# Optimization experiments

Hardware: AMD Instinct MI355X
Metric: run time of the kernel (lower is better)

Reference implementation:

```python
import jax, jax.numpy as jnp
import numpy as np

NUM_HEADS = 16

def setup_inputs() -> dict:
    key = jax.random.key(0)
    k1, k2, k3, k4 = jax.random.split(key, 4)
    B, N, C = 4, 2048, 1024
    x = jax.random.normal(k1, (B, N, C), dtype=jnp.float32)
    xpos = jax.random.randint(k2, (B, N), 0, 2048, dtype=jnp.int64)
    Wqkv = jax.random.normal(k3, (C, 3 * C), dtype=jnp.float32) * (C ** -0.5)
    Wproj = jax.random.normal(k4, (C, C), dtype=jnp.float32) * (C ** -0.5)
    bproj = jnp.zeros((C,), dtype=jnp.float32)
    return {"x": x, "xpos": xpos, "Wqkv": Wqkv, "Wproj": Wproj, "bproj": bproj}

def reference(x, xpos, Wqkv, Wproj, bproj):
    # rope is None in this configuration, so xpos is unused (matches torch default path).
    B, N, C = x.shape
    H = NUM_HEADS
    Dh = C // H
    scale = Dh ** -0.5
    qkv = jnp.einsum('bnc,cd->bnd', x, Wqkv)              # [B, N, 3C]
    qkv = qkv.reshape(B, N, 3, H, Dh)
    q, k, v = qkv[:, :, 0], qkv[:, :, 1], qkv[:, :, 2]    # [B, N, H, Dh]
    scores = jnp.einsum('bnhd,bmhd->bhnm', q, k) * scale  # [B, H, N, N]
    attn = jax.nn.softmax(scores, axis=-1)
    out = jnp.einsum('bhnm,bmhd->bnhd', attn, v)          # [B, N, H, Dh]
    out = out.reshape(B, N, C)
    return jnp.einsum('bnc,cd->bnd', out, Wproj) + bproj
```

## Files before the change

kernel.cpp:

```cpp
#include <hip/hip_runtime.h>
#include <stdint.h>

#define DEVINL __device__ __forceinline__

typedef __bf16 bf16x8 __attribute__((ext_vector_type(8)));
typedef float f32x4 __attribute__((ext_vector_type(4)));
typedef float f32x16 __attribute__((ext_vector_type(16)));
typedef uint32_t u32x4 __attribute__((ext_vector_type(4)));

DEVINL uint16_t f2bf(float f) {
    uint32_t u = __builtin_bit_cast(uint32_t, f);
    uint32_t r = (u + 0x7FFFu + ((u >> 16) & 1u)) >> 16;
    return (uint16_t)r;
}

DEVINL bf16x8 ld8(const uint16_t* p) {
    u32x4 v = *(const u32x4*)p;
    return __builtin_bit_cast(bf16x8, v);
}

DEVINL void gload16(const void* g, void* l) {
    __builtin_amdgcn_global_load_lds(
        (const __attribute__((address_space(1))) uint32_t*)g,
        (__attribute__((address_space(3))) uint32_t*)l, 16, 0, 0);
}

DEVINL uint32_t cvtpk(float lo, float hi) {
    uint32_t r;
    asm("v_cvt_pk_bf16_f32 %0, %1, %2" : "=v"(r) : "v"(lo), "v"(hi));
    return r;
}

DEVINL float exp2_fast(float x) {
    float r;
    asm("v_exp_f32 %0, %1" : "=v"(r) : "v"(x));
    return r;
}

DEVINL void transW_body(const float* __restrict__ W, uint16_t* __restrict__ WT,
                        int Nn, int n0, int k0, int tid, uint16_t* t) {
#pragma unroll
    for (int i = 0; i < 4; ++i) {
        int c = tid + i * 256;
        int kr = c >> 4, nc = c & 15;
        float4 v = *(const float4*)(W + (size_t)(k0 + kr) * Nn + n0 + nc * 4);
        t[(nc * 4 + 0) * 65 + kr] = f2bf(v.x);
        t[(nc * 4 + 1) * 65 + kr] = f2bf(v.y);
        t[(nc * 4 + 2) * 65 + kr] = f2bf(v.z);
        t[(nc * 4 + 3) * 65 + kr] = f2bf(v.w);
    }
    __syncthreads();
#pragma unroll
    for (int i = 0; i < 2; ++i) {
        int c = tid + i * 256;
        int nr = c >> 3, kc = c & 7;
        union { uint16_t u[8]; u32x4 v; } o;
#pragma unroll
        for (int j = 0; j < 8; ++j) o.u[j] = t[nr * 65 + kc * 8 + j];
        *(u32x4*)(WT + (size_t)(n0 + nr) * 1024 + k0 + kc * 8) = o.v;
    }
}

__global__ void k_prep(const float* __restrict__ x, uint16_t* __restrict__ xb,
                       const float* __restrict__ Wqkv, uint16_t* __restrict__ wqkvT,
                       const float* __restrict__ Wproj, uint16_t* __restrict__ wprojT) {
    __shared__ uint16_t t[64 * 65];
    int bid = blockIdx.x;
    int tid = threadIdx.x;
    if (bid < 4096) {
        int i = bid * 256 + tid;
        const float4* src = (const float4*)x + (size_t)i * 2;
        float4 a = src[0], b = src[1];
        union { uint16_t u[8]; u32x4 v; } o;
        o.u[0] = f2bf(a.x); o.u[1] = f2bf(a.y); o.u[2] = f2bf(a.z); o.u[3] = f2bf(a.w);
        o.u[4] = f2bf(b.x); o.u[5] = f2bf(b.y); o.u[6] = f2bf(b.z); o.u[7] = f2bf(b.w);
        ((u32x4*)xb)[i] = o.v;
    } else if (bid < 4864) {
        int idx = bid - 4096;
        transW_body(Wqkv, wqkvT, 3072, (idx % 48) * 64, (idx / 48) * 64, tid, t);
    } else {
        int idx = bid - 4864;
        transW_body(Wproj, wprojT, 1024, (idx % 16) * 64, (idx / 16) * 64, tid, t);
    }
}

__global__ void k_transV(const uint16_t* __restrict__ vn, uint16_t* __restrict__ vt) {
    __shared__ uint16_t t[64 * 65];
    int bh = blockIdx.y;
    int n0 = blockIdx.x * 64;
    int tid = threadIdx.x;
#pragma unroll
    for (int i = 0; i < 2; ++i) {
        int c = tid + i * 256;
        int n = c >> 3, dc = c & 7;
        u32x4 vv = *(const u32x4*)(vn + ((size_t)bh * 2048 + n0 + n) * 64 + dc * 8);
        union { u32x4 v4; uint16_t u[8]; } in; in.v4 = vv;
#pragma unroll
        for (int j = 0; j < 8; ++j) t[(dc * 8 + j) * 65 + n] = in.u[j];
    }
    __syncthreads();
#pragma unroll
    for (int i = 0; i < 2; ++i) {
        int c = tid + i * 256;
        int dh = c >> 3, nc = c & 7;
        union { uint16_t u[8]; u32x4 v4; } o;
#pragma unroll
        for (int j = 0; j < 8; ++j) o.u[j] = t[dh * 65 + nc * 8 + j];
        *(u32x4*)(vt + ((size_t)bh * 64 + dh) * 2048 + n0 + nc * 8) = o.v4;
    }
}

template <int MODE>
__global__ __launch_bounds__(256) void k_gemm(
    const uint16_t* __restrict__ A, const uint16_t* __restrict__ BT,
    const float* __restrict__ bias,
    uint16_t* __restrict__ qo, uint16_t* __restrict__ ko, uint16_t* __restrict__ vo,
    float* __restrict__ out) {
    __shared__ uint16_t a_lds[128 * 64];
    __shared__ uint16_t b_lds[128 * 64];
    int tid = threadIdx.x;
    int w = tid >> 6, l = tid & 63;
    int l15 = l & 15, l4 = l >> 4;
    int m0 = blockIdx.y * 128, n0 = blockIdx.x * 128;
    int wr = w >> 1, wc = w & 1;
    f32x4 acc[4][4] = {};

    for (int kt = 0; kt < 16; ++kt) {
#pragma unroll
        for (int i = 0; i < 4; ++i) {
            int c = i * 256 + w * 64 + l;
            int row = c >> 3, slot = c & 7;
            int kc = slot ^ (row & 7);
            gload16(A + (size_t)(m0 + row) * 1024 + kt * 64 + kc * 8,
                    a_lds + (size_t)(i * 256 + w * 64) * 8);
            gload16(BT + (size_t)(n0 + row) * 1024 + kt * 64 + kc * 8,
                    b_lds + (size_t)(i * 256 + w * 64) * 8);
        }
        __syncthreads();
#pragma unroll
        for (int kkk = 0; kkk < 2; ++kkk) {
            bf16x8 af[4], bfr[4];
#pragma unroll
            for (int i = 0; i < 4; ++i) {
                int row = wr * 64 + i * 16 + l15;
                af[i] = ld8(a_lds + row * 64 + ((kkk * 4 + l4) ^ (row & 7)) * 8);
                int rowb = wc * 64 + i * 16 + l15;
                bfr[i] = ld8(b_lds + rowb * 64 + ((kkk * 4 + l4) ^ (rowb & 7)) * 8);
            }
#pragma unroll
            for (int i = 0; i < 4; ++i)
#pragma unroll
                for (int j = 0; j < 4; ++j)
                    acc[i][j] = __builtin_amdgcn_mfma_f32_16x16x32_bf16(
                        af[i], bfr[j], acc[i][j], 0, 0, 0);
        }
        __syncthreads();
    }

    if constexpr (MODE == 0) {
#pragma unroll
        for (int i = 0; i < 4; ++i)
#pragma unroll
            for (int j = 0; j < 4; ++j) {
                int d = n0 + wc * 64 + j * 16 + l15;
                int s = d >> 10, h = (d >> 6) & 15, dh = d & 63;
                float sc = (s == 0) ? 0.18033688011112042f : 1.0f;
#pragma unroll
                for (int r = 0; r < 4; ++r) {
                    int m = m0 + wr * 64 + i * 16 + l4 * 4 + r;
                    int b = m >> 11, n = m & 2047;
                    int bh = b * 16 + h;
                    uint16_t val = f2bf(acc[i][j][r] * sc);
                    if (s == 1) {
                        ko[(size_t)bh * 131072 + (size_t)(n >> 6) * 4096 +
                           (dh >> 3) * 512 + (n & 63) * 8 + (dh & 7)] = val;
                    } else {
                        uint16_t* dst0 = (s == 0) ? qo : vo;
                        dst0[((size_t)bh * 2048 + n) * 64 + dh] = val;
                    }
                }
            }
    } else {
#pragma unroll
        for (int j = 0; j < 4; ++j) {
            int d = n0 + wc * 64 + j * 16 + l15;
            float bv = bias[d];
#pragma unroll
            for (int i = 0; i < 4; ++i)
#pragma unroll
                for (int r = 0; r < 4; ++r) {
                    int m = m0 + wr * 64 + i * 16 + l4 * 4 + r;
                    out[(size_t)m * 1024 + d] = acc[i][j][r] + bv;
                }
        }
    }
}

__global__ __launch_bounds__(256) void k_attn(
    const uint16_t* __restrict__ q, const uint16_t* __restrict__ kf_,
    const uint16_t* __restrict__ vt, uint16_t* __restrict__ o) {
    __shared__ uint16_t v_lds[2][64 * 64];
    int tid = threadIdx.x;
    int w = tid >> 6, l = tid & 63;
    int l31 = l & 31, g = l >> 5;
    int bid = blockIdx.x;
    int slot = bid >> 3;
    int bh = (bid & 7) * 8 + (slot >> 4);
    int qt = slot & 15;
    int qrow = qt * 128 + w * 32 + l31;
    const uint16_t* qb = q + ((size_t)bh * 2048 + qrow) * 64;
    const uint16_t* vbase = vt + (size_t)bh * 64 * 2048;
    const uint16_t* kfb = kf_ + (size_t)bh * 131072 + g * 512 + l31 * 8;

    bf16x8 qf[4];
#pragma unroll
    for (int kv = 0; kv < 4; ++kv) qf[kv] = ld8(qb + kv * 16 + g * 8);

    int c0 = w * 128 + l;
    int rr0 = c0 >> 3, sl0 = c0 & 7;
    int kc0 = sl0 ^ (rr0 & 7);
    int rr1 = rr0 + 8, kc1 = sl0 ^ (rr1 & 7);
    const uint16_t* vp0 = vbase + (size_t)rr0 * 2048 + kc0 * 8;
    const uint16_t* vp1 = vbase + (size_t)rr1 * 2048 + kc1 * 8;
    uint16_t* vd0 = v_lds[0] + w * 1024;
    uint16_t* vd1 = v_lds[1] + w * 1024;

    bf16x8 kr[8];
    auto loadK = [&](int t) {
        const uint16_t* p = kfb + (size_t)t * 4096;
        kr[0] = ld8(p);        kr[1] = ld8(p + 1024);
        kr[2] = ld8(p + 2048); kr[3] = ld8(p + 3072);
        kr[4] = ld8(p + 256);  kr[5] = ld8(p + 1280);
        kr[6] = ld8(p + 2304); kr[7] = ld8(p + 3328);
    };
    auto stageV = [&](uint16_t* vd) {
        gload16(vp0, vd); gload16(vp1, vd + 512);
        vp0 += 64; vp1 += 64;
    };

    f32x16 oa[2] = {};
    float lsum = 0.f;

    loadK(0);
    stageV(vd0);

    auto body = [&](int t, const uint16_t* vb, uint16_t* vdn) {
        asm volatile("s_barrier" ::: "memory");

        bf16x8 pfrag[4];
#pragma unroll
        for (int j = 0; j < 2; ++j) {
            f32x16 stj = {};
            __builtin_amdgcn_s_setprio(1);
#pragma unroll
            for (int kv = 0; kv < 4; ++kv)
                stj = __builtin_amdgcn_mfma_f32_32x32x16_bf16(kr[j * 4 + kv], qf[kv], stj, 0, 0, 0);
            __builtin_amdgcn_s_setprio(0);
            if (j == 1 && t < 31) {
                loadK(t + 1);
                stageV(vdn);
            }
#pragma unroll
            for (int h = 0; h < 2; ++h) {
                float e[8];
#pragma unroll
                for (int jj = 0; jj < 8; ++jj) e[jj] = exp2_fast(stj[h * 8 + jj]);
                lsum += ((e[0] + e[1]) + (e[2] + e[3])) + ((e[4] + e[5]) + (e[6] + e[7]));
                uint32_t a0 = cvtpk(e[0], e[1]), a1 = cvtpk(e[2], e[3]);
                uint32_t b0 = cvtpk(e[4], e[5]), b1 = cvtpk(e[6], e[7]);
                auto r0 = __builtin_amdgcn_permlane32_swap(a0, b0, false, false);
                auto r1 = __builtin_amdgcn_permlane32_swap(a1, b1, false, false);
                u32x4 f;
                f[0] = r0[0]; f[1] = r1[0]; f[2] = r0[1]; f[3] = r1[1];
                pfrag[j * 2 + h] = __builtin_bit_cast(bf16x8, f);
            }
        }

        if (t < 31) asm volatile("s_waitcnt vmcnt(10)\n\ts_barrier" ::: "memory");
        else        asm volatile("s_waitcnt vmcnt(0)\n\ts_barrier" ::: "memory");

        __builtin_amdgcn_s_setprio(1);
#pragma unroll
        for (int kv = 0; kv < 4; ++kv) {
#pragma unroll
            for (int dt = 0; dt < 2; ++dt) {
                int dh = dt * 32 + l31;
                bf16x8 vf = ld8(vb + dh * 64 + ((2 * kv + g) ^ (dh & 7)) * 8);
                oa[dt] = __builtin_amdgcn_mfma_f32_32x32x16_bf16(vf, pfrag[kv], oa[dt], 0, 0, 0);
            }
        }
        __builtin_amdgcn_s_setprio(0);
    };

    for (int kt = 0; kt < 32; kt += 2) {
        body(kt,     v_lds[0], vd1);
        body(kt + 1, v_lds[1], vd0);
    }

    float ltot = lsum + __shfl_xor(lsum, 32, 64);
    float inv = 1.0f / ltot;
    int b = bh >> 4, h = bh & 15;
    uint16_t* ob = o + ((size_t)(b * 2048 + qrow)) * 1024 + h * 64;
#pragma unroll
    for (int dt = 0; dt < 2; ++dt)
#pragma unroll
        for (int rq = 0; rq < 4; ++rq) {
            union { uint16_t u[4]; uint2 v; } pk;
#pragma unroll
            for (int rr = 0; rr < 4; ++rr) pk.u[rr] = f2bf(oa[dt][rq * 4 + rr] * inv);
            int dh0 = dt * 32 + rq * 8 + g * 4;
            *(uint2*)(ob + dh0) = pk.v;
        }
}

extern "C" void kernel_launch(void* const* d_in, const int* in_sizes, int n_in,
                              void* d_out, int out_size, void* d_ws, size_t ws_size,
                              hipStream_t stream) {
    const float* x     = (const float*)d_in[0];
    const float* Wqkv  = (const float*)d_in[2];
    const float* Wproj = (const float*)d_in[3];
    const float* bproj = (const float*)d_in[4];
    float* out = (float*)d_out;

    char* ws = (char*)d_ws;
    uint16_t* xb     = (uint16_t*)(ws);
    uint16_t* wqkvT  = (uint16_t*)(ws + 16777216);
    uint16_t* wprojT = (uint16_t*)(ws + 23068672);
    uint16_t* qws    = (uint16_t*)(ws + 25165824);
    uint16_t* kws    = (uint16_t*)(ws + 41943040);
    uint16_t* vT     = (uint16_t*)(ws + 58720256);
    uint16_t* vnat   = (uint16_t*)(ws + 75497472);
    uint16_t* attnout = xb;

    k_prep<<<dim3(5120), dim3(256), 0, stream>>>(x, xb, Wqkv, wqkvT, Wproj, wprojT);
    k_gemm<0><<<dim3(24, 64), dim3(256), 0, stream>>>(xb, wqkvT, nullptr, qws, kws, vnat, nullptr);
    k_transV<<<dim3(32, 64), dim3(256), 0, stream>>>(vnat, vT);
    k_attn<<<dim3(1024), dim3(256), 0, stream>>>(qws, kws, vT, attnout);
    k_gemm<1><<<dim3(8, 64), dim3(256), 0, stream>>>(attnout, wprojT, bproj, nullptr, nullptr, nullptr, out);
}
```

Before: 212.6 us.

## Write V in MFMA fragment layout from QKV GEMM and drop V transpose kernel

The QKV GEMM epilogue now writes V directly in a fragment-friendly layout with packed 8-byte stores, which removes the separate k_transV launch and its extra round-trip through memory. The attention kernel no longer stages V through LDS or uses barriers. Each wave loads K and V fragments straight from global memory into registers and walks 32-key tiles with a per-wave staggered start offset. In exchange, cross-wave reuse of V through shared memory is lost, so global and L2 traffic rises, and each tile's loads are less deeply prefetched.

Result: slower. 219.4 us (+3.2%).

```diff
diff --git a/kernel.cpp b/kernel.cpp
--- a/kernel.cpp
+++ b/kernel.cpp
@@ -84,32 +84,6 @@
     }
 }
 
-__global__ void k_transV(const uint16_t* __restrict__ vn, uint16_t* __restrict__ vt) {
-    __shared__ uint16_t t[64 * 65];
-    int bh = blockIdx.y;
-    int n0 = blockIdx.x * 64;
-    int tid = threadIdx.x;
-#pragma unroll
-    for (int i = 0; i < 2; ++i) {
-        int c = tid + i * 256;
-        int n = c >> 3, dc = c & 7;
-        u32x4 vv = *(const u32x4*)(vn + ((size_t)bh * 2048 + n0 + n) * 64 + dc * 8);
-        union { u32x4 v4; uint16_t u[8]; } in; in.v4 = vv;
-#pragma unroll
-        for (int j = 0; j < 8; ++j) t[(dc * 8 + j) * 65 + n] = in.u[j];
-    }
-    __syncthreads();
-#pragma unroll
-    for (int i = 0; i < 2; ++i) {
-        int c = tid + i * 256;
-        int dh = c >> 3, nc = c & 7;
-        union { uint16_t u[8]; u32x4 v4; } o;
-#pragma unroll
-        for (int j = 0; j < 8; ++j) o.u[j] = t[dh * 65 + nc * 8 + j];
-        *(u32x4*)(vt + ((size_t)bh * 64 + dh) * 2048 + n0 + nc * 8) = o.v4;
-    }
-}
-
 template <int MODE>
 __global__ __launch_bounds__(256) void k_gemm(
     const uint16_t* __restrict__ A, const uint16_t* __restrict__ BT,
@@ -165,18 +139,29 @@
                 int d = n0 + wc * 64 + j * 16 + l15;
                 int s = d >> 10, h = (d >> 6) & 15, dh = d & 63;
                 float sc = (s == 0) ? 0.18033688011112042f : 1.0f;
-#pragma unroll
-                for (int r = 0; r < 4; ++r) {
-                    int m = m0 + wr * 64 + i * 16 + l4 * 4 + r;
+                if (s == 2) {
+                    int m = m0 + wr * 64 + i * 16 + l4 * 4;
                     int b = m >> 11, n = m & 2047;
                     int bh = b * 16 + h;
-                    uint16_t val = f2bf(acc[i][j][r] * sc);
-                    if (s == 1) {
-                        ko[(size_t)bh * 131072 + (size_t)(n >> 6) * 4096 +
-                           (dh >> 3) * 512 + (n & 63) * 8 + (dh & 7)] = val;
-                    } else {
-                        uint16_t* dst0 = (s == 0) ? qo : vo;
-                        dst0[((size_t)bh * 2048 + n) * 64 + dh] = val;
+                    union { uint16_t u[4]; uint2 v2; } pk;
+#pragma unroll
+                    for (int r = 0; r < 4; ++r) pk.u[r] = f2bf(acc[i][j][r]);
+                    size_t addr = (size_t)bh * 131072 + (size_t)(n >> 5) * 2048 +
+                                  ((n & 31) >> 3) * 512 + dh * 8 + (n & 7);
+                    *(uint2*)(vo + addr) = pk.v2;
+                } else {
+#pragma unroll
+                    for (int r = 0; r < 4; ++r) {
+                        int m = m0 + wr * 64 + i * 16 + l4 * 4 + r;
+                        int b = m >> 11, n = m & 2047;
+                        int bh = b * 16 + h;
+                        uint16_t val = f2bf(acc[i][j][r] * sc);
+                        if (s == 1) {
+                            ko[(size_t)bh * 131072 + (size_t)(n >> 6) * 4096 +
+                               (dh >> 3) * 512 + (n & 63) * 8 + (dh & 7)] = val;
+                        } else {
+                            qo[((size_t)bh * 2048 + n) * 64 + dh] = val;
+                        }
                     }
                 }
             }
@@ -198,8 +183,7 @@
 
 __global__ __launch_bounds__(256) void k_attn(
     const uint16_t* __restrict__ q, const uint16_t* __restrict__ kf_,
-    const uint16_t* __restrict__ vt, uint16_t* __restrict__ o) {
-    __shared__ uint16_t v_lds[2][64 * 64];
+    const uint16_t* __restrict__ vf_, uint16_t* __restrict__ o) {
     int tid = threadIdx.x;
     int w = tid >> 6, l = tid & 63;
     int l31 = l & 31, g = l >> 5;
@@ -209,92 +193,65 @@
     int qt = slot & 15;
     int qrow = qt * 128 + w * 32 + l31;
     const uint16_t* qb = q + ((size_t)bh * 2048 + qrow) * 64;
-    const uint16_t* vbase = vt + (size_t)bh * 64 * 2048;
     const uint16_t* kfb = kf_ + (size_t)bh * 131072 + g * 512 + l31 * 8;
+    const uint16_t* vfb = vf_ + (size_t)bh * 131072 + g * 512 + l31 * 8;
 
     bf16x8 qf[4];
 #pragma unroll
     for (int kv = 0; kv < 4; ++kv) qf[kv] = ld8(qb + kv * 16 + g * 8);
 
-    int c0 = w * 128 + l;
-    int rr0 = c0 >> 3, sl0 = c0 & 7;
-    int kc0 = sl0 ^ (rr0 & 7);
-    int rr1 = rr0 + 8, kc1 = sl0 ^ (rr1 & 7);
-    const uint16_t* vp0 = vbase + (size_t)rr0 * 2048 + kc0 * 8;
-    const uint16_t* vp1 = vbase + (size_t)rr1 * 2048 + kc1 * 8;
-    uint16_t* vd0 = v_lds[0] + w * 1024;
-    uint16_t* vd1 = v_lds[1] + w * 1024;
-
-    bf16x8 kr[8];
+    bf16x8 kr[4];
+    bf16x8 vr[4];
+    f32x16 oa[2] = {};
+    float lsum = 0.f;
+
     auto loadK = [&](int t) {
-        const uint16_t* p = kfb + (size_t)t * 4096;
+        const uint16_t* p = kfb + (t >> 1) * 4096 + (t & 1) * 256;
         kr[0] = ld8(p);        kr[1] = ld8(p + 1024);
         kr[2] = ld8(p + 2048); kr[3] = ld8(p + 3072);
-        kr[4] = ld8(p + 256);  kr[5] = ld8(p + 1280);
-        kr[6] = ld8(p + 2304); kr[7] = ld8(p + 3328);
     };
-    auto stageV = [&](uint16_t* vd) {
-        gload16(vp0, vd); gload16(vp1, vd + 512);
-        vp0 += 64; vp1 += 64;
+    auto loadV = [&](int t) {
+        const uint16_t* p = vfb + t * 2048;
+        vr[0] = ld8(p);        vr[1] = ld8(p + 1024);
+        vr[2] = ld8(p + 256);  vr[3] = ld8(p + 1280);
     };
 
-    f32x16 oa[2] = {};
-    float lsum = 0.f;
-
-    loadK(0);
-    stageV(vd0);
-
-    auto body = [&](int t, const uint16_t* vb, uint16_t* vdn) {
-        asm volatile("s_barrier" ::: "memory");
-
-        bf16x8 pfrag[4];
-#pragma unroll
-        for (int j = 0; j < 2; ++j) {
-            f32x16 stj = {};
+    int start = w * 16;
+    loadK(start);
+    loadV(start);
+    int t = start;
+
+    for (int it = 0; it < 64; ++it) {
+        int tn = (t + 1) & 63;
+
+        f32x16 stj = {};
+        __builtin_amdgcn_s_setprio(1);
+#pragma unroll
+        for (int kv = 0; kv < 4; ++kv)
+            stj = __builtin_amdgcn_mfma_f32_32x32x16_bf16(kr[kv], qf[kv], stj, 0, 0, 0);
+        __builtin_amdgcn_s_setprio(0);
+        loadK(tn);
+
+#pragma unroll
+        for (int h = 0; h < 2; ++h) {
+            float e[8];
+#pragma unroll
+            for (int jj = 0; jj < 8; ++jj) e[jj] = exp2_fast(stj[h * 8 + jj]);
+            lsum += ((e[0] + e[1]) + (e[2] + e[3])) + ((e[4] + e[5]) + (e[6] + e[7]));
+            uint32_t a0 = cvtpk(e[0], e[1]), a1 = cvtpk(e[2], e[3]);
+            uint32_t b0 = cvtpk(e[4], e[5]), b1 = cvtpk(e[6], e[7]);
+            auto r0 = __builtin_amdgcn_permlane32_swap(a0, b0, false, false);
+            auto r1 = __builtin_amdgcn_permlane32_swap(a1, b1, false, false);
+            u32x4 f;
+            f[0] = r0[0]; f[1] = r1[0]; f[2] = r0[1]; f[3] = r1[1];
+            bf16x8 pf = __builtin_bit_cast(bf16x8, f);
             __builtin_amdgcn_s_setprio(1);
-#pragma unroll
-            for (int kv = 0; kv < 4; ++kv)
-                stj = __builtin_amdgcn_mfma_f32_32x32x16_bf16(kr[j * 4 + kv], qf[kv], stj, 0, 0, 0);
+            oa[0] = __builtin_amdgcn_mfma_f32_32x32x16_bf16(vr[h],     pf, oa[0], 0, 0, 0);
+            oa[1] = __builtin_amdgcn_mfma_f32_32x32x16_bf16(vr[2 + h], pf, oa[1], 0, 0, 0);
             __builtin_amdgcn_s_setprio(0);
-            if (j == 1 && t < 31) {
-                loadK(t + 1);
-                stageV(vdn);
-            }
-#pragma unroll
-            for (int h = 0; h < 2; ++h) {
-                float e[8];
-#pragma unroll
-                for (int jj = 0; jj < 8; ++jj) e[jj] = exp2_fast(stj[h * 8 + jj]);
-                lsum += ((e[0] + e[1]) + (e[2] + e[3])) + ((e[4] + e[5]) + (e[6] + e[7]));
-                uint32_t a0 = cvtpk(e[0], e[1]), a1 = cvtpk(e[2], e[3]);
-                uint32_t b0 = cvtpk(e[4], e[5]), b1 = cvtpk(e[6], e[7]);
-                auto r0 = __builtin_amdgcn_permlane32_swap(a0, b0, false, false);
-                auto r1 = __builtin_amdgcn_permlane32_swap(a1, b1, false, false);
-                u32x4 f;
-                f[0] = r0[0]; f[1] = r1[0]; f[2] = r0[1]; f[3] = r1[1];
-                pfrag[j * 2 + h] = __builtin_bit_cast(bf16x8, f);
-            }
-        }
-
-        if (t < 31) asm volatile("s_waitcnt vmcnt(10)\n\ts_barrier" ::: "memory");
-        else        asm volatile("s_waitcnt vmcnt(0)\n\ts_barrier" ::: "memory");
-
-        __builtin_amdgcn_s_setprio(1);
-#pragma unroll
-        for (int kv = 0; kv < 4; ++kv) {
-#pragma unroll
-            for (int dt = 0; dt < 2; ++dt) {
-                int dh = dt * 32 + l31;
-                bf16x8 vf = ld8(vb + dh * 64 + ((2 * kv + g) ^ (dh & 7)) * 8);
-                oa[dt] = __builtin_amdgcn_mfma_f32_32x32x16_bf16(vf, pfrag[kv], oa[dt], 0, 0, 0);
-            }
-        }
-        __builtin_amdgcn_s_setprio(0);
-    };
-
-    for (int kt = 0; kt < 32; kt += 2) {
-        body(kt,     v_lds[0], vd1);
-        body(kt + 1, v_lds[1], vd0);
+        }
+        loadV(tn);
+        t = tn;
     }
 
     float ltot = lsum + __shfl_xor(lsum, 32, 64);
@@ -328,13 +285,11 @@
     uint16_t* wprojT = (uint16_t*)(ws + 23068672);
     uint16_t* qws    = (uint16_t*)(ws + 25165824);
     uint16_t* kws    = (uint16_t*)(ws + 41943040);
-    uint16_t* vT     = (uint16_t*)(ws + 58720256);
-    uint16_t* vnat   = (uint16_t*)(ws + 75497472);
+    uint16_t* vfr    = (uint16_t*)(ws + 58720256);
     uint16_t* attnout = xb;
 
     k_prep<<<dim3(5120), dim3(256), 0, stream>>>(x, xb, Wqkv, wqkvT, Wproj, wprojT);
-    k_gemm<0><<<dim3(24, 64), dim3(256), 0, stream>>>(xb, wqkvT, nullptr, qws, kws, vnat, nullptr);
-    k_transV<<<dim3(32, 64), dim3(256), 0, stream>>>(vnat, vT);
-    k_attn<<<dim3(1024), dim3(256), 0, stream>>>(qws, kws, vT, attnout);
+    k_gemm<0><<<dim3(24, 64), dim3(256), 0, stream>>>(xb, wqkvT, nullptr, qws, kws, vfr, nullptr);
+    k_attn<<<dim3(1024), dim3(256), 0, stream>>>(qws, kws, vfr, attnout);
     k_gemm<1><<<dim3(8, 64), dim3(256), 0, stream>>>(attnout, wprojT, bproj, nullptr, nullptr, nullptr, out);
 }
```
